# Performance work log

Measured on AMD Instinct MI355X. Metric: run time of the kernel, lower is better.

## Reference

```python
import jax, jax.numpy as jnp
import numpy as np

B, N, T, F, HID, H = 128, 128, 12, 128, 256, 10


def setup_inputs() -> dict:
    key = jax.random.key(0)
    ks = jax.random.split(key, 8)
    s_in = 1.0 / np.sqrt(F)
    s_hid = 1.0 / np.sqrt(HID)
    return {
        "x": jax.random.normal(ks[0], (B, N, T, F), jnp.float32),
        "adj_weights": jax.random.normal(ks[1], (1, N, N), jnp.float32),
        "W1": jax.random.normal(ks[2], (F, HID), jnp.float32) * s_in,
        "b1": jnp.zeros((HID,), jnp.float32),
        "W2": jax.random.normal(ks[3], (HID, HID), jnp.float32) * s_hid,
        "b2": jnp.zeros((HID,), jnp.float32),
        "W3": jax.random.normal(ks[4], (HID, F), jnp.float32) * s_hid,
        "b3": jnp.zeros((F,), jnp.float32),
    }


def _graph_conv(x, norm_adj, W, b):
    # (B,N,N) @ (B,N,Fin) -> (B,N,Fin), then linear
    h = jnp.einsum("bnm,bmf->bnf", norm_adj, x)
    return h @ W + b


def reference(x, adj_weights, W1, b1, W2, b2, W3, b3):
    # initial state = last time step
    y0 = x[:, :, -1, :]                      # (B,N,F)
    adj = jax.nn.sigmoid(adj_weights)        # (1,N,N)
    adj = jnp.broadcast_to(adj, (x.shape[0], N, N))
    deg = jnp.clip(jnp.sum(adj, axis=-1, keepdims=True), 1.0, None)
    norm_adj = adj / deg                     # degree-normalized adjacency

    def f(y):
        h = jnp.tanh(_graph_conv(y, norm_adj, W1, b1))
        h = jnp.tanh(_graph_conv(h, norm_adj, W2, b2))
        return _graph_conv(h, norm_adj, W3, b3)

    # t = linspace(0, H, H) -> H points, dt = H/(H-1); torchdiffeq 'rk4'
    # uses the 3/8-rule alternative RK4 step (rk4_alt_step_func).
    dt = jnp.float32(H / (H - 1))

    def step(y, _):
        k1 = f(y)
        k2 = f(y + dt * k1 / 3.0)
        k3 = f(y + dt * (k2 - k1 / 3.0))
        k4 = f(y + dt * (k1 - k2 + k3))
        y1 = y + dt * (k1 + 3.0 * (k2 + k3) + k4) / 8.0
        return y1, y1

    _, ys = jax.lax.scan(step, y0, None, length=H - 1)  # (H-1,B,N,F)
    preds = jnp.concatenate([y0[None], ys], axis=0)      # (H,B,N,F)
    return jnp.transpose(preds, (1, 2, 0, 3))            # (B,N,H,F)
```

## Files before the change

kernel.cpp:

```cpp
#include <hip/hip_runtime.h>
#include <hip/hip_bf16.h>

typedef __attribute__((ext_vector_type(8))) short bf16x8;
typedef __attribute__((ext_vector_type(4))) float f32x4;
typedef unsigned short u16;
typedef unsigned int u32;

#define DT_ (10.0f / 9.0f)

__device__ __forceinline__ u16 f2bf(float f) {
  u32 u = __float_as_uint(f);
  u = (u + 0x7FFFu + ((u >> 16) & 1u)) >> 16;
  return (u16)u;
}

__device__ __forceinline__ u32 cvtpk(float lo, float hi) {
  __hip_bfloat162 h = __float22bfloat162_rn(float2{lo, hi});
  return *reinterpret_cast<u32*>(&h);
}

__device__ __forceinline__ float tanh_fast(float x) {
  float ax = fabsf(x);
  float e = __expf(-2.0f * ax);
  float t = (1.0f - e) * __builtin_amdgcn_rcpf(1.0f + e);
  return copysignf(t, x);
}

__device__ __forceinline__ bf16x8 frag_lds(const u16* Mb, int row0, int kE, int strideB) {
  const int l = threadIdx.x & 63;
  const int r = row0 + (l & 15);
  const int kb = (kE + ((l >> 4) << 3)) << 1;
  const int off = r * strideB + (kb ^ ((r & 7) << 4));
  return *(const bf16x8*)((const char*)Mb + off);
}

__device__ __forceinline__ bf16x8 frag_glb(const u16* WT, int col0, int kE, int K) {
  const int l = threadIdx.x & 63;
  const int j = col0 + (l & 15);
  const int k = kE + ((l >> 4) << 3);
  return *(const bf16x8*)(WT + j * K + k);
}

template <int KST, bool BLDS>
__device__ __forceinline__ void gemm2(f32x4 (&acc)[4][2], const u16* Ab, int aStrideB, int mb,
                                      const u16* Bp, int bK, int nb) {
#pragma unroll
  for (int mt = 0; mt < 4; ++mt)
#pragma unroll
    for (int nt = 0; nt < 2; ++nt) acc[mt][nt] = (f32x4){0.f, 0.f, 0.f, 0.f};
  bf16x8 av0[4], bv0[2], av1[4], bv1[2];
#pragma unroll
  for (int nt = 0; nt < 2; ++nt) {
    if constexpr (BLDS) bv0[nt] = frag_lds(Bp, nb + nt * 16, 0, 256);
    else                bv0[nt] = frag_glb(Bp, nb + nt * 16, 0, bK);
  }
#pragma unroll
  for (int mt = 0; mt < 4; ++mt) av0[mt] = frag_lds(Ab, mb + mt * 16, 0, aStrideB);
#pragma unroll 1
  for (int ks = 0; ks < KST; ks += 2) {
    const int k1 = (ks + 1) * 32;
#pragma unroll
    for (int nt = 0; nt < 2; ++nt) {
      if constexpr (BLDS) bv1[nt] = frag_lds(Bp, nb + nt * 16, k1, 256);
      else                bv1[nt] = frag_glb(Bp, nb + nt * 16, k1, bK);
    }
#pragma unroll
    for (int mt = 0; mt < 4; ++mt) av1[mt] = frag_lds(Ab, mb + mt * 16, k1, aStrideB);
#pragma unroll
    for (int nt = 0; nt < 2; ++nt)
#pragma unroll
      for (int mt = 0; mt < 4; ++mt)
        acc[mt][nt] = __builtin_amdgcn_mfma_f32_16x16x32_bf16(av0[mt], bv0[nt], acc[mt][nt], 0, 0, 0);
    if (ks + 2 < KST) {
      const int k2 = (ks + 2) * 32;
#pragma unroll
      for (int nt = 0; nt < 2; ++nt) {
        if constexpr (BLDS) bv0[nt] = frag_lds(Bp, nb + nt * 16, k2, 256);
        else                bv0[nt] = frag_glb(Bp, nb + nt * 16, k2, bK);
      }
#pragma unroll
      for (int mt = 0; mt < 4; ++mt) av0[mt] = frag_lds(Ab, mb + mt * 16, k2, aStrideB);
    }
#pragma unroll
    for (int nt = 0; nt < 2; ++nt)
#pragma unroll
      for (int mt = 0; mt < 4; ++mt)
        acc[mt][nt] = __builtin_amdgcn_mfma_f32_16x16x32_bf16(av1[mt], bv1[nt], acc[mt][nt], 0, 0, 0);
  }
}

template <int KST, bool BLDS>
__device__ __forceinline__ void gemm1(f32x4 (&acc)[4], const u16* Ab, int aStrideB, int mb,
                                      const u16* Bp, int bK, int nb) {
#pragma unroll
  for (int mt = 0; mt < 4; ++mt) acc[mt] = (f32x4){0.f, 0.f, 0.f, 0.f};
  bf16x8 av0[4], av1[4];
  bf16x8 bv0, bv1;
  if constexpr (BLDS) bv0 = frag_lds(Bp, nb, 0, 256);
  else                bv0 = frag_glb(Bp, nb, 0, bK);
#pragma unroll
  for (int mt = 0; mt < 4; ++mt) av0[mt] = frag_lds(Ab, mb + mt * 16, 0, aStrideB);
#pragma unroll 1
  for (int ks = 0; ks < KST; ks += 2) {
    const int k1 = (ks + 1) * 32;
    if constexpr (BLDS) bv1 = frag_lds(Bp, nb, k1, 256);
    else                bv1 = frag_glb(Bp, nb, k1, bK);
#pragma unroll
    for (int mt = 0; mt < 4; ++mt) av1[mt] = frag_lds(Ab, mb + mt * 16, k1, aStrideB);
#pragma unroll
    for (int mt = 0; mt < 4; ++mt)
      acc[mt] = __builtin_amdgcn_mfma_f32_16x16x32_bf16(av0[mt], bv0, acc[mt], 0, 0, 0);
    if (ks + 2 < KST) {
      const int k2 = (ks + 2) * 32;
      if constexpr (BLDS) bv0 = frag_lds(Bp, nb, k2, 256);
      else                bv0 = frag_glb(Bp, nb, k2, bK);
#pragma unroll
      for (int mt = 0; mt < 4; ++mt) av0[mt] = frag_lds(Ab, mb + mt * 16, k2, aStrideB);
    }
#pragma unroll
    for (int mt = 0; mt < 4; ++mt)
      acc[mt] = __builtin_amdgcn_mfma_f32_16x16x32_bf16(av1[mt], bv1, acc[mt], 0, 0, 0);
  }
}

__device__ __forceinline__ void epi_T2(const f32x4 (&acc)[4][2], u16* Q, int nb, int mb, int lane) {
  const int l15 = lane & 15, lg = lane >> 4;
#pragma unroll
  for (int nt = 0; nt < 2; ++nt) {
    const int c = nb + nt * 16 + l15;
    const int swz = (c & 7) << 4;
    char* rowp = (char*)Q + c * 256;
#pragma unroll
    for (int mt = 0; mt < 4; ++mt) {
      f32x4 v = acc[mt][nt];
      const int r0 = mb + mt * 16 + (lg << 2);
      uint2 pk;
      pk.x = cvtpk(v.x, v.y);
      pk.y = cvtpk(v.z, v.w);
      *(uint2*)(rowp + ((r0 << 1) ^ swz)) = pk;
    }
  }
}

__device__ __forceinline__ void epi_H2(const f32x4 (&acc)[4][2], u16* P, const float* __restrict__ b,
                                       int nb, int mb, int lane) {
  const int l15 = lane & 15, lg = lane >> 4;
#pragma unroll
  for (int nt = 0; nt < 2; ++nt) {
    const int c = nb + nt * 16 + l15;
    const float bb = b[c];
    const int csh = c << 1;
#pragma unroll
    for (int mt = 0; mt < 4; ++mt) {
      f32x4 v = acc[mt][nt];
      const int r0 = mb + mt * 16 + (lg << 2);
      float t0 = tanh_fast(v.x + bb), t1 = tanh_fast(v.y + bb);
      float t2 = tanh_fast(v.z + bb), t3 = tanh_fast(v.w + bb);
      const u32 p01 = cvtpk(t0, t1);
      const u32 p23 = cvtpk(t2, t3);
      *(u16*)((char*)P + (r0 + 0) * 512 + (csh ^ (((r0 + 0) & 7) << 4))) = (u16)p01;
      *(u16*)((char*)P + (r0 + 1) * 512 + (csh ^ (((r0 + 1) & 7) << 4))) = (u16)(p01 >> 16);
      *(u16*)((char*)P + (r0 + 2) * 512 + (csh ^ (((r0 + 2) & 7) << 4))) = (u16)p23;
      *(u16*)((char*)P + (r0 + 3) * 512 + (csh ^ (((r0 + 3) & 7) << 4))) = (u16)(p23 >> 16);
    }
  }
}

template <int E>
__device__ __forceinline__ void feval(int step,
    u16* P, u16* Q, const u16* As,
    const u16* __restrict__ W1T, const u16* __restrict__ W2T, const u16* __restrict__ W3T,
    const float* __restrict__ b1, const float* __restrict__ b2, const float* __restrict__ b3,
    f32x4* __restrict__ SA, f32x4* __restrict__ SB,
    float* __restrict__ out,
    int batch, int tid, int lane, int mb, int wn) {
  const int l15 = lane & 15, lg = lane >> 4;

#pragma unroll 1
  for (int h = 0; h < 2; ++h) {
    f32x4 acc[4][2];
    gemm2<4, false>(acc, P, 256, mb, W1T, 128, wn * 64 + h * 32);
    epi_T2(acc, Q, wn * 64 + h * 32, mb, lane);
  }
  __syncthreads();
#pragma unroll 1
  for (int h = 0; h < 2; ++h) {
    f32x4 acc[4][2];
    gemm2<4, true>(acc, As, 256, mb, Q, 0, wn * 64 + h * 32);
    epi_H2(acc, P, b1, wn * 64 + h * 32, mb, lane);
  }
  __syncthreads();
#pragma unroll 1
  for (int h = 0; h < 2; ++h) {
    f32x4 acc[4][2];
    gemm2<8, false>(acc, P, 512, mb, W2T, 256, wn * 64 + h * 32);
    epi_T2(acc, Q, wn * 64 + h * 32, mb, lane);
  }
  __syncthreads();
#pragma unroll 1
  for (int h = 0; h < 2; ++h) {
    f32x4 acc[4][2];
    gemm2<4, true>(acc, As, 256, mb, Q, 0, wn * 64 + h * 32);
    epi_H2(acc, P, b2, wn * 64 + h * 32, mb, lane);
  }
  __syncthreads();
  {
    f32x4 acc[4][2];
    gemm2<8, false>(acc, P, 512, mb, W3T, 256, wn * 32);
    epi_T2(acc, Q, wn * 32, mb, lane);
  }
  __syncthreads();

#pragma unroll 1
  for (int p = 0; p < 2; ++p) {
    f32x4 ya[4], ba[4];
#pragma unroll
    for (int q = 0; q < 4; ++q) ya[q] = SA[(p * 4 + q) * 512 + tid];
    if constexpr (E == 2 || E == 3) {
#pragma unroll
      for (int q = 0; q < 4; ++q) ba[q] = SB[(p * 4 + q) * 512 + tid];
    }
    f32x4 acc[4];
    gemm1<4, true>(acc, As, 256, mb, Q, 0, wn * 32 + p * 16);
    const int c = wn * 32 + p * 16 + l15;
    const float bb = b3[c];
    const int cz = c << 1;
#pragma unroll
    for (int mt = 0; mt < 4; ++mt) {
      f32x4 v = acc[mt];
      const int r0 = mb + mt * 16 + (lg << 2);
      const int i4 = p * 4 + mt;
      f32x4 wa, wb, zv;
#pragma unroll
      for (int e = 0; e < 4; ++e) {
        const int r = r0 + e;
        const float kv = v[e] + bb;
        float z;
        if constexpr (E == 1) {
          wb[e] = kv;
          z = ya[mt][e] + (DT_ * (1.0f / 3.0f)) * kv;
        } else if constexpr (E == 2) {
          const float k1 = ba[mt][e];
          const float y = ya[mt][e];
          z = y + DT_ * (kv - k1 * (1.0f / 3.0f));
          wb[e] = y + DT_ * (k1 - kv);
          wa[e] = y + (DT_ * 0.125f) * (k1 + 3.0f * kv);
        } else if constexpr (E == 3) {
          z = ba[mt][e] + DT_ * kv;
          wa[e] = ya[mt][e] + (DT_ * 0.375f) * kv;
        } else {
          const float yn = ya[mt][e] + (DT_ * 0.125f) * kv;
          wa[e] = yn;
          __builtin_nontemporal_store(yn, &out[batch * 163840 + r * 1280 + (step + 1) * 128 + c]);
          z = yn;
        }
        zv[e] = z;
      }
      const u32 z01 = cvtpk(zv.x, zv.y);
      const u32 z23 = cvtpk(zv.z, zv.w);
      *(u16*)((char*)P + (r0 + 0) * 256 + (cz ^ (((r0 + 0) & 7) << 4))) = (u16)z01;
      *(u16*)((char*)P + (r0 + 1) * 256 + (cz ^ (((r0 + 1) & 7) << 4))) = (u16)(z01 >> 16);
      *(u16*)((char*)P + (r0 + 2) * 256 + (cz ^ (((r0 + 2) & 7) << 4))) = (u16)z23;
      *(u16*)((char*)P + (r0 + 3) * 256 + (cz ^ (((r0 + 3) & 7) << 4))) = (u16)(z23 >> 16);
      if constexpr (E == 1 || E == 2) SB[i4 * 512 + tid] = wb;
      if constexpr (E != 1) SA[i4 * 512 + tid] = wa;
    }
  }
  __syncthreads();
}

__global__ __launch_bounds__(512, 2)
void ode_main(
    const u16* __restrict__ Aswz,
    const u16* __restrict__ W1T, const u16* __restrict__ W2T, const u16* __restrict__ W3T,
    const float* __restrict__ b1, const float* __restrict__ b2, const float* __restrict__ b3,
    const float* __restrict__ x,
    f32x4* __restrict__ KS,
    float* __restrict__ out) {
  __shared__ u16 P[32768];
  __shared__ u16 Q[32768];
  __shared__ u16 As[16384];
  const int tid = threadIdx.x;
  const int lane = tid & 63;
  const int wid = tid >> 6;
  const int wm = wid >> 2, wn = wid & 3;
  const int mb = wm * 64;
  const int l15 = lane & 15, lg = lane >> 4;
  const int batch = blockIdx.x;
  f32x4* SA = KS + batch * 8192;
  f32x4* SB = SA + 4096;

  {
    const uint4* s = (const uint4*)Aswz;
    uint4* d = (uint4*)As;
#pragma unroll
    for (int i = 0; i < 4; ++i) d[tid + i * 512] = s[tid + i * 512];
  }

#pragma unroll 1
  for (int p = 0; p < 2; ++p)
#pragma unroll 1
    for (int mt = 0; mt < 4; ++mt) {
      const int c = wn * 32 + p * 16 + l15;
      f32x4 w;
#pragma unroll
      for (int e = 0; e < 4; ++e) {
        const int r = mb + mt * 16 + (lg << 2) + e;
        const float v = x[((batch * 128 + r) * 12 + 11) * 128 + c];
        w[e] = v;
        __builtin_nontemporal_store(v, &out[batch * 163840 + r * 1280 + c]);
        *(u16*)((char*)P + r * 256 + ((c << 1) ^ ((r & 7) << 4))) = f2bf(v);
      }
      SA[(p * 4 + mt) * 512 + tid] = w;
    }
  __syncthreads();

  for (int s = 0; s < 9; ++s) {
    feval<1>(s, P, Q, As, W1T, W2T, W3T, b1, b2, b3, SA, SB, out, batch, tid, lane, mb, wn);
    feval<2>(s, P, Q, As, W1T, W2T, W3T, b1, b2, b3, SA, SB, out, batch, tid, lane, mb, wn);
    feval<3>(s, P, Q, As, W1T, W2T, W3T, b1, b2, b3, SA, SB, out, batch, tid, lane, mb, wn);
    feval<4>(s, P, Q, As, W1T, W2T, W3T, b1, b2, b3, SA, SB, out, batch, tid, lane, mb, wn);
  }
}


__global__ void prep_adj_k(const float* __restrict__ adjw, u16* __restrict__ Aswz) {
  const int n = blockIdx.x;
  const int m = threadIdx.x;
  const float w = adjw[n * 128 + m];
  const float sg = 1.0f / (1.0f + __expf(-w));
  float s = sg;
#pragma unroll
  for (int o = 1; o < 64; o <<= 1) s += __shfl_xor(s, o);
  __shared__ float red[2];
  if ((m & 63) == 0) red[m >> 6] = s;
  __syncthreads();
  const float deg = fmaxf(red[0] + red[1], 1.0f);
  const float v = sg / deg;
  *(u16*)((char*)Aswz + n * 256 + ((m << 1) ^ ((n & 7) << 4))) = f2bf(v);
}

__global__ void prep_w_k(const float* __restrict__ W1, const float* __restrict__ W2,
                         const float* __restrict__ W3,
                         u16* __restrict__ W1T, u16* __restrict__ W2T, u16* __restrict__ W3T) {
  const int i = blockIdx.x * 256 + threadIdx.x;
  if (i < 32768) {
    W1T[i] = f2bf(W1[(i & 127) * 256 + (i >> 7)]);
    W3T[i] = f2bf(W3[(i & 255) * 128 + (i >> 8)]);
  }
  if (i < 65536) W2T[i] = f2bf(W2[(i & 255) * 256 + (i >> 8)]);
}

extern "C" void kernel_launch(void* const* d_in, const int* in_sizes, int n_in,
                              void* d_out, int out_size, void* d_ws, size_t ws_size,
                              hipStream_t stream) {
  const float* x    = (const float*)d_in[0];
  const float* adjw = (const float*)d_in[1];
  const float* W1   = (const float*)d_in[2];
  const float* b1   = (const float*)d_in[3];
  const float* W2   = (const float*)d_in[4];
  const float* b2   = (const float*)d_in[5];
  const float* W3   = (const float*)d_in[6];
  const float* b3   = (const float*)d_in[7];
  float* out = (float*)d_out;

  u16* Aswz = (u16*)d_ws;
  u16* W1T = Aswz + 16384;
  u16* W2T = W1T + 32768;
  u16* W3T = W2T + 65536;
  f32x4* KS = (f32x4*)(W3T + 32768);

  prep_adj_k<<<128, 128, 0, stream>>>(adjw, Aswz);
  prep_w_k<<<256, 256, 0, stream>>>(W1, W2, W3, W1T, W2T, W3T);
  ode_main<<<128, 512, 0, stream>>>(Aswz, W1T, W2T, W3T, b1, b2, b3, x, KS, out);
}
```

Measured before the change: 982.0 us.

## Reorder first graph conv to aggregate before projecting with W1

The first layer now computes (A·y)·W1 instead of A·(y·W1). The adjacency GEMM runs on the 128-wide input rather than the 256-wide projected features, which halves that GEMM's work. The stage output z is stored transposed (feature-major) in the upper half of Q so it can feed the adjacency GEMM directly, and stores are packed into 8-byte writes. One extra rounding to bf16 happens on the aggregated input, and the shared-memory buffer roles change, so aliasing between Q and Qhi has to stay correct.

```diff
diff --git a/kernel.cpp b/kernel.cpp
--- a/kernel.cpp
+++ b/kernel.cpp
@@ -138,6 +138,26 @@
       pk.x = cvtpk(v.x, v.y);
       pk.y = cvtpk(v.z, v.w);
       *(uint2*)(rowp + ((r0 << 1) ^ swz)) = pk;
+    }
+  }
+}
+
+__device__ __forceinline__ void epi_N2(const f32x4 (&acc)[4][2], u16* Qlo, int nb, int mb, int lane) {
+  const int l15 = lane & 15, lg = lane >> 4;
+#pragma unroll
+  for (int nt = 0; nt < 2; ++nt) {
+    const int c = nb + nt * 16 + l15;
+    const int csh = c << 1;
+#pragma unroll
+    for (int mt = 0; mt < 4; ++mt) {
+      f32x4 v = acc[mt][nt];
+      const int r0 = mb + mt * 16 + (lg << 2);
+      const u32 p01 = cvtpk(v.x, v.y);
+      const u32 p23 = cvtpk(v.z, v.w);
+      *(u16*)((char*)Qlo + (r0 + 0) * 256 + (csh ^ (((r0 + 0) & 7) << 4))) = (u16)p01;
+      *(u16*)((char*)Qlo + (r0 + 1) * 256 + (csh ^ (((r0 + 1) & 7) << 4))) = (u16)(p01 >> 16);
+      *(u16*)((char*)Qlo + (r0 + 2) * 256 + (csh ^ (((r0 + 2) & 7) << 4))) = (u16)p23;
+      *(u16*)((char*)Qlo + (r0 + 3) * 256 + (csh ^ (((r0 + 3) & 7) << 4))) = (u16)(p23 >> 16);
     }
   }
 }
@@ -175,18 +195,18 @@
     float* __restrict__ out,
     int batch, int tid, int lane, int mb, int wn) {
   const int l15 = lane & 15, lg = lane >> 4;
-
+  u16* Qhi = Q + 16384;
+
+  {
+    f32x4 acc[4][2];
+    gemm2<4, true>(acc, As, 256, mb, Qhi, 0, wn * 32);
+    epi_N2(acc, Q, wn * 32, mb, lane);
+  }
+  __syncthreads();
 #pragma unroll 1
   for (int h = 0; h < 2; ++h) {
     f32x4 acc[4][2];
-    gemm2<4, false>(acc, P, 256, mb, W1T, 128, wn * 64 + h * 32);
-    epi_T2(acc, Q, wn * 64 + h * 32, mb, lane);
-  }
-  __syncthreads();
-#pragma unroll 1
-  for (int h = 0; h < 2; ++h) {
-    f32x4 acc[4][2];
-    gemm2<4, true>(acc, As, 256, mb, Q, 0, wn * 64 + h * 32);
+    gemm2<4, false>(acc, Q, 256, mb, W1T, 128, wn * 64 + h * 32);
     epi_H2(acc, P, b1, wn * 64 + h * 32, mb, lane);
   }
   __syncthreads();
@@ -224,7 +244,8 @@
     gemm1<4, true>(acc, As, 256, mb, Q, 0, wn * 32 + p * 16);
     const int c = wn * 32 + p * 16 + l15;
     const float bb = b3[c];
-    const int cz = c << 1;
+    const int swz = (c & 7) << 4;
+    char* zrow = (char*)Qhi + c * 256;
 #pragma unroll
     for (int mt = 0; mt < 4; ++mt) {
       f32x4 v = acc[mt];
@@ -256,12 +277,10 @@
         }
         zv[e] = z;
       }
-      const u32 z01 = cvtpk(zv.x, zv.y);
-      const u32 z23 = cvtpk(zv.z, zv.w);
-      *(u16*)((char*)P + (r0 + 0) * 256 + (cz ^ (((r0 + 0) & 7) << 4))) = (u16)z01;
-      *(u16*)((char*)P + (r0 + 1) * 256 + (cz ^ (((r0 + 1) & 7) << 4))) = (u16)(z01 >> 16);
-      *(u16*)((char*)P + (r0 + 2) * 256 + (cz ^ (((r0 + 2) & 7) << 4))) = (u16)z23;
-      *(u16*)((char*)P + (r0 + 3) * 256 + (cz ^ (((r0 + 3) & 7) << 4))) = (u16)(z23 >> 16);
+      uint2 pk;
+      pk.x = cvtpk(zv.x, zv.y);
+      pk.y = cvtpk(zv.z, zv.w);
+      *(uint2*)(zrow + ((r0 << 1) ^ swz)) = pk;
       if constexpr (E == 1 || E == 2) SB[i4 * 512 + tid] = wb;
       if constexpr (E != 1) SA[i4 * 512 + tid] = wa;
     }
@@ -289,6 +308,7 @@
   const int batch = blockIdx.x;
   f32x4* SA = KS + batch * 8192;
   f32x4* SB = SA + 4096;
+  u16* Qhi = Q + 16384;
 
   {
     const uint4* s = (const uint4*)Aswz;
@@ -302,15 +322,19 @@
 #pragma unroll 1
     for (int mt = 0; mt < 4; ++mt) {
       const int c = wn * 32 + p * 16 + l15;
+      const int r0 = mb + mt * 16 + (lg << 2);
       f32x4 w;
 #pragma unroll
       for (int e = 0; e < 4; ++e) {
-        const int r = mb + mt * 16 + (lg << 2) + e;
+        const int r = r0 + e;
         const float v = x[((batch * 128 + r) * 12 + 11) * 128 + c];
         w[e] = v;
         __builtin_nontemporal_store(v, &out[batch * 163840 + r * 1280 + c]);
-        *(u16*)((char*)P + r * 256 + ((c << 1) ^ ((r & 7) << 4))) = f2bf(v);
       }
+      uint2 pk;
+      pk.x = cvtpk(w.x, w.y);
+      pk.y = cvtpk(w.z, w.w);
+      *(uint2*)((char*)Qhi + c * 256 + ((r0 << 1) ^ ((c & 7) << 4))) = pk;
       SA[(p * 4 + mt) * 512 + tid] = w;
     }
   __syncthreads();
```

After: 942.5 us. 4.0% less time.
